# Kernel tuning notes

Hardware: AMD Instinct MI355X
Metric: run time of the kernel (lower is better)

The kernel has to match this reference:

```python
import jax, jax.numpy as jnp
import numpy as np

B, S, D = 4, 1024, 768
H = 12
DK = D // H            # 64
NUM_EMB = 10
MAX_DIST = 100000.0 * 2 ** 0.5
POS_SCALE = 100000.0   # tile positions live in [0, 100000]


def setup_inputs() -> dict:
    key = jax.random.key(0)
    ks = jax.random.split(key, 12)
    query = jax.random.normal(ks[0], (B, S, D), dtype=jnp.float32)
    key_t = jax.random.normal(ks[1], (B, S, D), dtype=jnp.float32)
    value = jax.random.normal(ks[2], (B, S, D), dtype=jnp.float32)
    tile_positions = jax.random.uniform(ks[3], (B, S, 2), dtype=jnp.float32) * POS_SCALE
    # Linear weights, torch layout [out, in]; xavier_uniform init, zero bias
    lim = float(np.sqrt(6.0 / (D + D)))
    Wq = jax.random.uniform(ks[4], (D, D), minval=-lim, maxval=lim, dtype=jnp.float32)
    Wk = jax.random.uniform(ks[5], (D, D), minval=-lim, maxval=lim, dtype=jnp.float32)
    Wv = jax.random.uniform(ks[6], (D, D), minval=-lim, maxval=lim, dtype=jnp.float32)
    bq = jnp.zeros((D,), jnp.float32)
    bk = jnp.zeros((D,), jnp.float32)
    bv = jnp.zeros((D,), jnp.float32)
    emb_k = jax.random.normal(ks[7], (NUM_EMB, DK), dtype=jnp.float32)  # nn.Embedding default N(0,1)
    return {"query": query, "key": key_t, "value": value,
            "tile_positions": tile_positions,
            "Wq": Wq, "bq": bq, "Wk": Wk, "bk": bk, "Wv": Wv, "bv": bv,
            "emb_k": emb_k}


def reference(query, key, value, tile_positions, Wq, bq, Wk, bk, Wv, bv, emb_k):
    b, s, _ = query.shape
    # projections -> [B, H, S, DK]
    q = (query @ Wq.T + bq).reshape(b, s, H, DK).transpose(0, 2, 1, 3)
    k = (key   @ Wk.T + bk).reshape(b, s, H, DK).transpose(0, 2, 1, 3)
    v = (value @ Wv.T + bv).reshape(b, s, H, DK).transpose(0, 2, 1, 3)
    # pairwise distances, normalized, discretized to embedding indices
    pos = jax.lax.stop_gradient(tile_positions)
    diff = pos[:, :, None, :] - pos[:, None, :, :]          # [B,S,S,2]
    dist = jnp.sqrt(jnp.sum(diff * diff, axis=-1)) / MAX_DIST  # [B,S,S]
    idx = jnp.clip(jnp.round(dist * (NUM_EMB - 1)), 0, NUM_EMB - 1).astype(jnp.int32)
    rk = emb_k[idx]                                          # [B,S,S,DK]
    # logits: QK^T plus distance-aware key bias
    attn_logits = jnp.einsum('bhqd,bhkd->bhqk', q, k)
    attn_logits = attn_logits + jnp.einsum('bhqd,bqkd->bhqk', q, rk)
    attn_logits = attn_logits / (DK ** 0.5)
    attention = jax.nn.softmax(attn_logits, axis=-1)
    out = jnp.einsum('bhqk,bhkd->bhqd', attention, v)       # [B,H,S,DK]
    out = out.transpose(0, 2, 1, 3).reshape(b, s, -1)       # [B,S,D]
    return out
```

## Files before the change

### kernel.cpp

```cpp
#include <hip/hip_runtime.h>
#include <hip/hip_bf16.h>

#define Bsz 4
#define Ssz 1024
#define Dsz 768
#define Hn 12
#define DKsz 64
#define NUMEMB 10

#define IDX_OFF 64
#define K_OFF   4194368
#define V_OFF   10485824
#define WBF_OFF 16777280
#define XBF_OFF 20316224
#define WS_TIER_B 20316224ULL
#define WS_TIER_A 39190592ULL

#define NXz 3145728
#define NWz 589824

#define KVBUF 4096

typedef __attribute__((ext_vector_type(8))) short short8;
typedef __attribute__((ext_vector_type(8))) float float8;
typedef __attribute__((ext_vector_type(4))) float f32x4;
typedef __attribute__((ext_vector_type(4))) unsigned int u32x4;
typedef __attribute__((ext_vector_type(2))) unsigned int u32x2;
typedef __attribute__((ext_vector_type(4))) short s16x4;

__device__ __forceinline__ float bfbits2f(short u) {
    union { unsigned int i; float f; } v;
    v.i = ((unsigned int)(unsigned short)u) << 16;
    return v.f;
}
__device__ __forceinline__ unsigned short f2bf_bits(float f) {
    __hip_bfloat16 h = __float2bfloat16(f);
    return *reinterpret_cast<unsigned short*>(&h);
}

__device__ __forceinline__ int dtvote(const unsigned int* p, int n) {
    int cnt = 0;
    for (int i = (threadIdx.x & 63); i < n; i += 64) {
        const unsigned int ex = (p[i] >> 7) & 0xFF;
        cnt += (ex >= 110 && ex <= 145) ? 1 : 0;
    }
#pragma unroll
    for (int off = 1; off < 64; off <<= 1) cnt += __shfl_xor(cnt, off, 64);
    return (2 * cnt > n) ? 1 : 0;
}

template<bool BF16>
__device__ __forceinline__ float loadf(const void* base, size_t idx) {
    if constexpr (BF16) return __bfloat162float(((const __hip_bfloat16*)base)[idx]);
    else return ((const float*)base)[idx];
}
template<bool BF16>
__device__ __forceinline__ short8 load8bf(const void* base, size_t idx) {
    if constexpr (BF16) {
        return *(const short8*)((const short*)base + idx);
    } else {
        float8 f = *(const float8*)((const float*)base + idx);
        short8 r;
#pragma unroll
        for (int i = 0; i < 8; i++) r[i] = (short)f2bf_bits(f[i]);
        return r;
    }
}
template<bool BF16>
__device__ __forceinline__ float8 load8f(const void* base, size_t idx) {
    if constexpr (BF16) {
        short8 s = *(const short8*)((const short*)base + idx);
        float8 f;
#pragma unroll
        for (int i = 0; i < 8; i++) f[i] = bfbits2f(s[i]);
        return f;
    } else {
        return *(const float8*)((const float*)base + idx);
    }
}

template<bool PB>
__device__ __forceinline__ void idx_body(
    const void* pos, unsigned char* __restrict__ idxb, int kt, int qt, int b)
{
    const int t = threadIdx.x;
    const int r = t >> 2, cc = t & 3;
    const int q = qt * 64 + r;
    const float qx = loadf<PB>(pos, ((size_t)b * Ssz + q) * 2);
    const float qy = loadf<PB>(pos, ((size_t)b * Ssz + q) * 2 + 1);
    const float MAXD = 141421.35623730951f;
    const int k0 = kt * 64 + cc * 16;
    unsigned int w[4];
#pragma unroll
    for (int g = 0; g < 4; g++) {
        unsigned int acc = 0;
#pragma unroll
        for (int u = 0; u < 4; u++) {
            const int k = k0 + g * 4 + u;
            const float kx = loadf<PB>(pos, ((size_t)b * Ssz + k) * 2);
            const float ky = loadf<PB>(pos, ((size_t)b * Ssz + k) * 2 + 1);
            const float dx = __fsub_rn(qx, kx);
            const float dy = __fsub_rn(qy, ky);
            const float ss = __fadd_rn(__fmul_rn(dx, dx), __fmul_rn(dy, dy));
            const float dist = __fdiv_rn(sqrtf(ss), MAXD);
            const float d9 = __fmul_rn(dist, 9.0f);
            int idx = (int)rintf(d9);
            idx = idx < 0 ? 0 : (idx > NUMEMB - 1 ? NUMEMB - 1 : idx);
            acc |= ((unsigned int)idx) << (8 * u);
        }
        w[g] = acc;
    }
    u32x4 v; v[0] = w[0]; v[1] = w[1]; v[2] = w[2]; v[3] = w[3];
    *(u32x4*)(idxb + ((size_t)(b * Ssz + q)) * Ssz + k0) = v;
}

__global__ __launch_bounds__(64) void detect_kernel(
    const unsigned int* __restrict__ q, const unsigned int* __restrict__ p,
    const unsigned int* __restrict__ w, const unsigned int* __restrict__ e,
    int* __restrict__ flags)
{
    const int which = blockIdx.x;
    const unsigned int* ptr = (which == 0) ? q : ((which == 1) ? p : ((which == 2) ? w : e));
    const int n = (which == 3) ? 320 : ((which == 1) ? 4096 : 1024);
    const int f = dtvote(ptr, n);
    if (threadIdx.x == 0) flags[which] = f;
}

__global__ __launch_bounds__(256) void idx_kernel(
    const void* pos, const int* __restrict__ flags, unsigned char* __restrict__ idxb)
{
    if (flags[1] != 0) idx_body<true >(pos, idxb, blockIdx.x, blockIdx.y, blockIdx.z);
    else               idx_body<false>(pos, idxb, blockIdx.x, blockIdx.y, blockIdx.z);
}

__global__ __launch_bounds__(256) void prep_kernel(
    const void* __restrict__ X0, const void* __restrict__ X1, const void* __restrict__ X2,
    const void* __restrict__ W0, const void* __restrict__ W1, const void* __restrict__ W2,
    const void* __restrict__ tpos, const void* __restrict__ emb,
    int* __restrict__ flags, short* __restrict__ Xbf, short* __restrict__ Wbf,
    unsigned char* __restrict__ idxb, int nconv, int doX)
{
    if ((int)blockIdx.x >= nconv) {
        const int i = blockIdx.x - nconv;
        const int kt = i & 15, qt = (i >> 4) & 15, b = i >> 8;
        const int pb = dtvote((const unsigned int*)tpos, 1024);
        if (pb) idx_body<true >(tpos, idxb, kt, qt, b);
        else    idx_body<false>(tpos, idxb, kt, qt, b);
        return;
    }

    if (blockIdx.x == 1) {
        const int f = dtvote((const unsigned int*)tpos, 1024);
        if (threadIdx.x == 0) flags[1] = f;
    } else if (blockIdx.x == 3) {
        const int f = dtvote((const unsigned int*)emb, 320);
        if (threadIdx.x == 0) flags[3] = f;
    }
    const bool xb = dtvote((const unsigned int*)X0, 256) != 0;
    const bool wb = dtvote((const unsigned int*)W0, 256) != 0;
    if (blockIdx.x == 0 && threadIdx.x == 0) { flags[0] = xb ? 1 : 0; flags[2] = wb ? 1 : 0; }

    const long t = (long)blockIdx.x * 256 + threadIdx.x;
    if (doX) {
        const long i8 = t * 8;
        if (i8 < (long)3 * NXz) {
            const int z = (int)(i8 / NXz);
            const long off = i8 - (long)z * NXz;
            const void* X = (z == 0) ? X0 : ((z == 1) ? X1 : X2);
            short8 v = xb ? load8bf<true>(X, off) : load8bf<false>(X, off);
            *(short8*)(Xbf + i8) = v;
        } else {
            const long j = i8 - (long)3 * NXz;
            const int z = (int)(j / NWz);
            const long off = j - (long)z * NWz;
            const void* W = (z == 0) ? W0 : ((z == 1) ? W1 : W2);
            short8 v = wb ? load8bf<true>(W, off) : load8bf<false>(W, off);
            *(short8*)(Wbf + j) = v;
        }
    } else {
        const long j = t * 8;
        const int z = (int)(j / NWz);
        const long off = j - (long)z * NWz;
        const void* W = (z == 0) ? W0 : ((z == 1) ? W1 : W2);
        short8 v = wb ? load8bf<true>(W, off) : load8bf<false>(W, off);
        *(short8*)(Wbf + j) = v;
    }
}

template<bool XB, bool WB>
__device__ __forceinline__ void proj_body(
    const void* X, const void* W, const void* bias, bool biasbf, void* Y, bool ybf,
    int zmode, int bx, int by, short* As, short* Bs)
{
    const int tid  = threadIdx.x;
    const int wave = tid >> 6;
    const int lane = tid & 63;
    const int l15  = lane & 15;
    const int quad = lane >> 4;
    const int wm = wave & 1;
    const int wn = wave >> 1;
    const int m0 = bx * 64;
    const int n0 = by * 128;

    f32x4 acc[2][4];
#pragma unroll
    for (int i = 0; i < 2; i++)
#pragma unroll
        for (int j = 0; j < 4; j++) acc[i][j] = (f32x4)0.0f;

    const int r0 = tid >> 3;
    const int cc = tid & 7;

    short8 pa0 = load8bf<XB>(X, (size_t)(m0 + r0)      * Dsz + cc * 8);
    short8 pa1 = load8bf<XB>(X, (size_t)(m0 + 32 + r0) * Dsz + cc * 8);
    short8 pb0 = load8bf<WB>(W, (size_t)(n0 + r0)      * Dsz + cc * 8);
    short8 pb1 = load8bf<WB>(W, (size_t)(n0 + 32 + r0) * Dsz + cc * 8);
    short8 pb2 = load8bf<WB>(W, (size_t)(n0 + 64 + r0) * Dsz + cc * 8);
    short8 pb3 = load8bf<WB>(W, (size_t)(n0 + 96 + r0) * Dsz + cc * 8);

    for (int kk = 0; kk < Dsz; kk += 64) {
        __syncthreads();
        *(short8*)&As[(r0)      * 72 + cc * 8] = pa0;
        *(short8*)&As[(32 + r0) * 72 + cc * 8] = pa1;
        *(short8*)&Bs[(r0)      * 72 + cc * 8] = pb0;
        *(short8*)&Bs[(32 + r0) * 72 + cc * 8] = pb1;
        *(short8*)&Bs[(64 + r0) * 72 + cc * 8] = pb2;
        *(short8*)&Bs[(96 + r0) * 72 + cc * 8] = pb3;
        __syncthreads();

        if (kk + 64 < Dsz) {
            const int k2 = kk + 64 + cc * 8;
            pa0 = load8bf<XB>(X, (size_t)(m0 + r0)      * Dsz + k2);
            pa1 = load8bf<XB>(X, (size_t)(m0 + 32 + r0) * Dsz + k2);
            pb0 = load8bf<WB>(W, (size_t)(n0 + r0)      * Dsz + k2);
            pb1 = load8bf<WB>(W, (size_t)(n0 + 32 + r0) * Dsz + k2);
            pb2 = load8bf<WB>(W, (size_t)(n0 + 64 + r0) * Dsz + k2);
            pb3 = load8bf<WB>(W, (size_t)(n0 + 96 + r0) * Dsz + k2);
        }

#pragma unroll
        for (int st = 0; st < 2; st++) {
            short8 af[2], bf[4];
#pragma unroll
            for (int i = 0; i < 2; i++)
                af[i] = *(const short8*)&As[(wm * 32 + i * 16 + l15) * 72 + st * 32 + quad * 8];
#pragma unroll
            for (int j = 0; j < 4; j++)
                bf[j] = *(const short8*)&Bs[(wn * 64 + j * 16 + l15) * 72 + st * 32 + quad * 8];
#pragma unroll
            for (int i = 0; i < 2; i++)
#pragma unroll
                for (int j = 0; j < 4; j++)
                    acc[i][j] = __builtin_amdgcn_mfma_f32_16x16x32_bf16(af[i], bf[j], acc[i][j], 0, 0, 0);
        }
    }

#pragma unroll
    for (int j = 0; j < 4; j++) {
        const int n = n0 + wn * 64 + j * 16 + l15;
        const float bv_ = biasbf ? loadf<true>(bias, n) : loadf<false>(bias, n);
        const int hh = n >> 6, dk = n & 63;
#pragma unroll
        for (int i = 0; i < 2; i++) {
            const int ms = m0 + wm * 32 + i * 16 + quad * 4;
            const int bb = ms >> 10;
            const int s0 = ms & 1023;
            if (zmode == 2) {
                s16x4 pkv;
#pragma unroll
                for (int r = 0; r < 4; r++) pkv[r] = (short)f2bf_bits(acc[i][j][r] + bv_);
                *(s16x4*)((short*)Y + (((size_t)bb * Hn + hh) * DKsz + dk) * Ssz + s0) = pkv;
            } else if (zmode == 1) {
#pragma unroll
                for (int r = 0; r < 4; r++)
                    ((__hip_bfloat16*)Y)[(((size_t)bb * Hn + hh) * Ssz + (s0 + r)) * DKsz + dk] =
                        __float2bfloat16(acc[i][j][r] + bv_);
            } else {
#pragma unroll
                for (int r = 0; r < 4; r++) {
                    const float val = acc[i][j][r] + bv_;
                    const size_t oi = (size_t)(ms + r) * Dsz + n;
                    if (ybf) ((__hip_bfloat16*)Y)[oi] = __float2bfloat16(val);
                    else     ((float*)Y)[oi] = val;
                }
            }
        }
    }
}

__global__ __launch_bounds__(256) void proj_kernel(
    const void* X0, const void* X1, const void* X2,
    const void* Wq, const void* bq, const void* Wk, const void* bk,
    const void* Wv, const void* bv,
    void* Qw, void* Kw, void* Vw, const int* __restrict__ flags,
    int fx, int fw)
{
    __shared__ __align__(16) short As[64 * 72];
    __shared__ __align__(16) short Bs[128 * 72];
    const int z = blockIdx.z;
    const void* X = (z == 0) ? X0 : ((z == 1) ? X1 : X2);
    const void* W = (z == 0) ? Wq : ((z == 1) ? Wk : Wv);
    const void* B = (z == 0) ? bq : ((z == 1) ? bk : bv);
    void* Y = (z == 0) ? Qw : ((z == 1) ? Kw : Vw);
    const bool xb = fx || flags[0] != 0;
    const bool wb = fw || flags[2] != 0;
    const bool biasbf = flags[2] != 0;
    const bool ybf = (flags[0] != 0) || (z != 0);
    if (xb) { if (wb) proj_body<true , true >(X, W, B, biasbf, Y, ybf, z, blockIdx.x, blockIdx.y, As, Bs);
              else    proj_body<true , false>(X, W, B, biasbf, Y, ybf, z, blockIdx.x, blockIdx.y, As, Bs); }
    else    { if (wb) proj_body<false, true >(X, W, B, biasbf, Y, ybf, z, blockIdx.x, blockIdx.y, As, Bs);
              else    proj_body<false, false>(X, W, B, biasbf, Y, ybf, z, blockIdx.x, blockIdx.y, As, Bs); }
}

template<bool QB, bool EB>
__device__ __forceinline__ void attn_body(
    const void* Qw, const short* __restrict__ Ks, const short* __restrict__ Vs,
    const unsigned char* __restrict__ idxb, const void* __restrict__ emb, void* out,
    unsigned short* Klds, unsigned short* Vtlds, float* qe)
{
    const int linear = blockIdx.x + 16 * (blockIdx.y + Hn * blockIdx.z);
    const int work = (linear & 7) * 96 + (linear >> 3);
    const int qt = work & 15;
    const int bh = work >> 4;
    const int h = bh % Hn;
    const int b = bh / Hn;

    const int tid  = threadIdx.x;
    const int wave = tid >> 6;
    const int lane = tid & 63;
    const int l15  = lane & 15;
    const int quad = lane >> 4;

    const float CSC = 0.18033688011112042f;

    for (int p = tid; p < 64 * NUMEMB; p += 256) {
        const int row = p / NUMEMB, e = p - row * NUMEMB;
        const size_t qoff = ((size_t)b * Ssz + qt * 64 + row) * Dsz + h * DKsz;
        float s = 0.f;
#pragma unroll
        for (int c = 0; c < 8; c++) {
            short8 qv = load8bf<QB>(Qw, qoff + c * 8);
            float8 ef = load8f<EB>(emb, (size_t)e * DKsz + c * 8);
#pragma unroll
            for (int i = 0; i < 8; i++) s += bfbits2f(qv[i]) * ef[i];
        }
        qe[p] = s * CSC;
    }

    short8 qfrag[2];
    {
        const size_t qbase = ((size_t)b * Ssz + qt * 64 + wave * 16 + l15) * Dsz + h * DKsz;
        qfrag[0] = load8bf<QB>(Qw, qbase + quad * 8);
        qfrag[1] = load8bf<QB>(Qw, qbase + 32 + quad * 8);
    }

    float m_run = -1e30f, l_run = 0.f;
    f32x4 oacc[4];
#pragma unroll
    for (int j = 0; j < 4; j++) oacc[j] = (f32x4)0.0f;

    const int r0 = tid >> 3, cc = tid & 7;
    const int swr   = (r0 & 3) | (((r0 >> 3) & 1) << 2);
    const int wroff = r0 * 64 + (cc ^ swr) * 8;

    const int swk = (l15 & 3) | (((l15 >> 2) & 1) << 2);
    const int vsw = (l15 & 3) | (((l15 >> 3) & 1) << 2);
    int koff[4][2];
#pragma unroll
    for (int jb = 0; jb < 4; jb++) {
        const int krow = (jb & 2) * 16 + (l15 >> 2) * 8 + (jb & 1) * 4 + (l15 & 3);
#pragma unroll
        for (int st = 0; st < 2; st++)
            koff[jb][st] = krow * 64 + ((st * 4 + quad) ^ swk) * 8;
    }
    int voff[2];
#pragma unroll
    for (int st = 0; st < 2; st++) voff[st] = ((st * 4 + quad) ^ vsw) * 8;

    const short* kp = Ks + ((size_t)(b * Hn + h) * Ssz) * DKsz + tid * 8;
    const short* vp = Vs + ((size_t)(b * Hn + h) * DKsz + r0) * Ssz + cc * 8;
    const unsigned char* ip = idxb + ((size_t)b * Ssz + qt * 64 + wave * 16 + l15) * Ssz + quad * 8;
    const int qrow10 = (wave * 16 + l15) * NUMEMB;

    short8 pk0 = *(const short8*)(kp);
    short8 pk1 = *(const short8*)(kp + 2048);
    short8 pv0 = *(const short8*)(vp);
    short8 pv1 = *(const short8*)(vp + 32 * Ssz);
    u32x2 idA = *(const u32x2*)(ip);
    u32x2 idB = *(const u32x2*)(ip + 32);

    *(short8*)&Klds[wroff]            = pk0;
    *(short8*)&Klds[32 * 64 + wroff]  = pk1;
    *(short8*)&Vtlds[wroff]           = pv0;
    *(short8*)&Vtlds[32 * 64 + wroff] = pv1;
    __syncthreads();

    for (int it = 0; it < 16; ++it) {
        const int cur = (it & 1) * KVBUF;
        const int nxt = cur ^ KVBUF;
        const unsigned int jd[4] = { idA[0], idA[1], idB[0], idB[1] };

        if (it + 1 < 16) {
            kp += 4096;
            vp += 64;
            ip += 64;
            pk0 = *(const short8*)(kp);
            pk1 = *(const short8*)(kp + 2048);
            pv0 = *(const short8*)(vp);
            pv1 = *(const short8*)(vp + 32 * Ssz);
            idA = *(const u32x2*)(ip);
            idB = *(const u32x2*)(ip + 32);
        }

        f32x4 sf[4];
#pragma unroll
        for (int jb = 0; jb < 4; jb++) sf[jb] = (f32x4)0.0f;
        __builtin_amdgcn_s_setprio(1);
#pragma unroll
        for (int st = 0; st < 2; st++) {
#pragma unroll
            for (int jb = 0; jb < 4; jb++) {
                short8 kf = *(const short8*)&Klds[cur + koff[jb][st]];
                sf[jb] = __builtin_amdgcn_mfma_f32_16x16x32_bf16(kf, qfrag[st], sf[jb], 0, 0, 0);
            }
        }
        __builtin_amdgcn_s_setprio(0);

        float sv[4][4];
#pragma unroll
        for (int jb = 0; jb < 4; jb++) {
            const unsigned int iw = jd[jb];
#pragma unroll
            for (int r = 0; r < 4; r++)
                sv[jb][r] = fmaf(sf[jb][r], CSC, qe[qrow10 + ((iw >> (8 * r)) & 0xFF)]);
        }

        float t0 = fmaxf(fmaxf(sv[0][0], sv[0][1]), fmaxf(sv[0][2], sv[0][3]));
        float t1 = fmaxf(fmaxf(sv[1][0], sv[1][1]), fmaxf(sv[1][2], sv[1][3]));
        float t2 = fmaxf(fmaxf(sv[2][0], sv[2][1]), fmaxf(sv[2][2], sv[2][3]));
        float t3 = fmaxf(fmaxf(sv[3][0], sv[3][1]), fmaxf(sv[3][2], sv[3][3]));
        float vmax = fmaxf(fmaxf(t0, t1), fmaxf(t2, t3));
        vmax = fmaxf(vmax, __shfl_xor(vmax, 16, 64));
        vmax = fmaxf(vmax, __shfl_xor(vmax, 32, 64));

        if (!__all(vmax - m_run <= 8.0f)) {
            const float mnew = fmaxf(m_run, vmax);
            const float alpha = exp2f(m_run - mnew);
            m_run = mnew;
            l_run *= alpha;
            float aO[4];
#pragma unroll
            for (int r = 0; r < 4; r++)
                aO[r] = __shfl(alpha, (lane & 48) | (quad * 4 + r), 64);
#pragma unroll
            for (int j = 0; j < 4; j++) {
                f32x4 o = oacc[j];
#pragma unroll
                for (int r = 0; r < 4; r++) o[r] *= aO[r];
                oacc[j] = o;
            }
        }

#pragma unroll
        for (int jb = 0; jb < 4; jb++)
#pragma unroll
            for (int r = 0; r < 4; r++)
                sv[jb][r] = exp2f(sv[jb][r] - m_run);

        float s0 = (sv[0][0] + sv[0][1]) + (sv[0][2] + sv[0][3]);
        float s1 = (sv[1][0] + sv[1][1]) + (sv[1][2] + sv[1][3]);
        float s2 = (sv[2][0] + sv[2][1]) + (sv[2][2] + sv[2][3]);
        float s3 = (sv[3][0] + sv[3][1]) + (sv[3][2] + sv[3][3]);
        float psum = (s0 + s1) + (s2 + s3);
        psum += __shfl_xor(psum, 16, 64);
        psum += __shfl_xor(psum, 32, 64);
        l_run += psum;

        short8 pa[2];
#pragma unroll
        for (int st = 0; st < 2; st++)
#pragma unroll
            for (int j = 0; j < 8; j++)
                pa[st][j] = (short)f2bf_bits(sv[2 * st + (j >> 2)][j & 3]);

        __builtin_amdgcn_s_setprio(1);
#pragma unroll
        for (int st = 0; st < 2; st++) {
#pragma unroll
            for (int j = 0; j < 4; j++) {
                short8 vb = *(const short8*)&Vtlds[cur + (j * 16 + l15) * 64 + voff[st]];
                oacc[j] = __builtin_amdgcn_mfma_f32_16x16x32_bf16(pa[st], vb, oacc[j], 0, 0, 0);
            }
        }
        __builtin_amdgcn_s_setprio(0);

        if (it + 1 < 16) {
            *(short8*)&Klds[nxt + wroff]            = pk0;
            *(short8*)&Klds[nxt + 32 * 64 + wroff]  = pk1;
            *(short8*)&Vtlds[nxt + wroff]           = pv0;
            *(short8*)&Vtlds[nxt + 32 * 64 + wroff] = pv1;
        }
        __syncthreads();
    }

    const float inv = 1.0f / l_run;
    float invO[4];
#pragma unroll
    for (int r = 0; r < 4; r++)
        invO[r] = __shfl(inv, (lane & 48) | (quad * 4 + r), 64);

#pragma unroll
    for (int r = 0; r < 4; r++) {
        const int m = qt * 64 + wave * 16 + quad * 4 + r;
#pragma unroll
        for (int j = 0; j < 4; j++) {
            const int n = h * DKsz + j * 16 + l15;
            const float val = oacc[j][r] * invO[r];
            const size_t oidx = ((size_t)b * Ssz + m) * Dsz + n;
            if constexpr (QB) ((__hip_bfloat16*)out)[oidx] = __float2bfloat16(val);
            else              ((float*)out)[oidx] = val;
        }
    }
}

__global__ __launch_bounds__(256) void attn_kernel(
    const void* Qw, const short* __restrict__ Ks, const short* __restrict__ Vs,
    const unsigned char* __restrict__ idxb, const void* __restrict__ emb, void* out,
    const int* __restrict__ flags)
{
    __shared__ __align__(16) unsigned short Klds[2 * KVBUF];
    __shared__ __align__(16) unsigned short Vtlds[2 * KVBUF];
    __shared__ __align__(16) float qe[64 * NUMEMB];

    const bool qb = flags[0] != 0, eb = flags[3] != 0;
    if (qb) { if (eb) attn_body<true , true >(Qw, Ks, Vs, idxb, emb, out, Klds, Vtlds, qe);
              else    attn_body<true , false>(Qw, Ks, Vs, idxb, emb, out, Klds, Vtlds, qe); }
    else    { if (eb) attn_body<false, true >(Qw, Ks, Vs, idxb, emb, out, Klds, Vtlds, qe);
              else    attn_body<false, false>(Qw, Ks, Vs, idxb, emb, out, Klds, Vtlds, qe); }
}

extern "C" void kernel_launch(void* const* d_in, const int* in_sizes, int n_in,
                              void* d_out, int out_size, void* d_ws, size_t ws_size,
                              hipStream_t stream) {
    const void* query = d_in[0];
    const void* key   = d_in[1];
    const void* value = d_in[2];
    const void* tpos  = d_in[3];
    const void* Wq    = d_in[4];
    const void* bq    = d_in[5];
    const void* Wk    = d_in[6];
    const void* bk    = d_in[7];
    const void* Wv    = d_in[8];
    const void* bv    = d_in[9];
    const void* emb   = d_in[10];

    int*           flags = (int*)d_ws;
    unsigned char* idxb  = (unsigned char*)d_ws + IDX_OFF;
    void*          Kw    = (char*)d_ws + K_OFF;
    void*          Vw    = (char*)d_ws + V_OFF;
    short*         Wbf   = (short*)((char*)d_ws + WBF_OFF);
    short*         Xbf   = (short*)((char*)d_ws + XBF_OFF);
    void*          Qw    = d_out;

    const bool tierA = ws_size >= WS_TIER_A;
    const bool tierB = !tierA && ws_size >= WS_TIER_B;

    if (tierA) {
        prep_kernel<<<5472 + 1024, 256, 0, stream>>>(
            query, key, value, Wq, Wk, Wv, tpos, emb,
            flags, Xbf, Wbf, idxb, 5472, 1);
        proj_kernel<<<dim3(64, 6, 3), 256, 0, stream>>>(
            Xbf, Xbf + NXz, Xbf + 2 * NXz,
            Wbf, bq, Wbf + NWz, bk, Wbf + 2 * NWz, bv,
            Qw, Kw, Vw, flags, 1, 1);
    } else if (tierB) {
        prep_kernel<<<864 + 1024, 256, 0, stream>>>(
            query, key, value, Wq, Wk, Wv, tpos, emb,
            flags, Xbf, Wbf, idxb, 864, 0);
        proj_kernel<<<dim3(64, 6, 3), 256, 0, stream>>>(
            query, key, value,
            Wbf, bq, Wbf + NWz, bk, Wbf + 2 * NWz, bv,
            Qw, Kw, Vw, flags, 0, 1);
    } else {
        detect_kernel<<<4, 64, 0, stream>>>(
            (const unsigned int*)query, (const unsigned int*)tpos,
            (const unsigned int*)Wq, (const unsigned int*)emb, flags);
        idx_kernel<<<dim3(16, 16, Bsz), 256, 0, stream>>>(tpos, flags, idxb);
        proj_kernel<<<dim3(64, 6, 3), 256, 0, stream>>>(
            query, key, value, Wq, bq, Wk, bk, Wv, bv,
            Qw, Kw, Vw, flags, 0, 0);
    }

    attn_kernel<<<dim3(16, Hn, Bsz), 256, 0, stream>>>(
        Qw, (const short*)Kw, (const short*)Vw, idxb, emb, d_out, flags);
}
```

Measured before the change: 200.9 us.

## Split attention KV range across two wave groups with LDS merge

The attention block grows to 512 threads, split into two groups of four waves. Each group processes half of the key/value sequence, so a block runs 8 iterations instead of 16. The groups merge their partial online-softmax state (max, sum, output) through shared memory in a final combine step. Double buffering is replaced by single-buffered per-group LDS with two barriers per iteration. The change trades per-block latency against the extra merge work, the extra synchronisation, and the loss of load/compute overlap.

```diff
diff --git a/kernel.cpp b/kernel.cpp
--- a/kernel.cpp
+++ b/kernel.cpp
@@ -19,7 +19,7 @@
 #define NXz 3145728
 #define NWz 589824
 
-#define KVBUF 4096
+#define POOLSZ 17664
 
 typedef __attribute__((ext_vector_type(8))) short short8;
 typedef __attribute__((ext_vector_type(8))) float float8;
@@ -316,7 +316,7 @@
 __device__ __forceinline__ void attn_body(
     const void* Qw, const short* __restrict__ Ks, const short* __restrict__ Vs,
     const unsigned char* __restrict__ idxb, const void* __restrict__ emb, void* out,
-    unsigned short* Klds, unsigned short* Vtlds, float* qe)
+    unsigned short* pool)
 {
     const int linear = blockIdx.x + 16 * (blockIdx.y + Hn * blockIdx.z);
     const int work = (linear & 7) * 96 + (linear >> 3);
@@ -327,13 +327,19 @@
 
     const int tid  = threadIdx.x;
     const int wave = tid >> 6;
+    const int g    = wave >> 2;
+    const int wv   = wave & 3;
     const int lane = tid & 63;
     const int l15  = lane & 15;
     const int quad = lane >> 4;
 
+    unsigned short* Klds  = pool + g * 8192;
+    unsigned short* Vtlds = pool + g * 8192 + 4096;
+    float* qe = (float*)(pool + 16384);
+
     const float CSC = 0.18033688011112042f;
 
-    for (int p = tid; p < 64 * NUMEMB; p += 256) {
+    for (int p = tid; p < 64 * NUMEMB; p += 512) {
         const int row = p / NUMEMB, e = p - row * NUMEMB;
         const size_t qoff = ((size_t)b * Ssz + qt * 64 + row) * Dsz + h * DKsz;
         float s = 0.f;
@@ -349,7 +355,7 @@
 
     short8 qfrag[2];
     {
-        const size_t qbase = ((size_t)b * Ssz + qt * 64 + wave * 16 + l15) * Dsz + h * DKsz;
+        const size_t qbase = ((size_t)b * Ssz + qt * 64 + wv * 16 + l15) * Dsz + h * DKsz;
         qfrag[0] = load8bf<QB>(Qw, qbase + quad * 8);
         qfrag[1] = load8bf<QB>(Qw, qbase + 32 + quad * 8);
     }
@@ -359,7 +365,8 @@
 #pragma unroll
     for (int j = 0; j < 4; j++) oacc[j] = (f32x4)0.0f;
 
-    const int r0 = tid >> 3, cc = tid & 7;
+    const int tg = tid & 255;
+    const int r0 = tg >> 3, cc = tg & 7;
     const int swr   = (r0 & 3) | (((r0 >> 3) & 1) << 2);
     const int wroff = r0 * 64 + (cc ^ swr) * 8;
 
@@ -377,10 +384,11 @@
 #pragma unroll
     for (int st = 0; st < 2; st++) voff[st] = ((st * 4 + quad) ^ vsw) * 8;
 
-    const short* kp = Ks + ((size_t)(b * Hn + h) * Ssz) * DKsz + tid * 8;
-    const short* vp = Vs + ((size_t)(b * Hn + h) * DKsz + r0) * Ssz + cc * 8;
-    const unsigned char* ip = idxb + ((size_t)b * Ssz + qt * 64 + wave * 16 + l15) * Ssz + quad * 8;
-    const int qrow10 = (wave * 16 + l15) * NUMEMB;
+    const short* kp = Ks + ((size_t)(b * Hn + h) * Ssz + g * 512) * DKsz + tg * 8;
+    const short* vp = Vs + ((size_t)(b * Hn + h) * DKsz + r0) * Ssz + g * 512 + cc * 8;
+    const unsigned char* ip = idxb + ((size_t)b * Ssz + qt * 64 + wv * 16 + l15) * Ssz
+                                   + g * 512 + quad * 8;
+    const int qrow10 = (wv * 16 + l15) * NUMEMB;
 
     short8 pk0 = *(const short8*)(kp);
     short8 pk1 = *(const short8*)(kp + 2048);
@@ -393,14 +401,12 @@
     *(short8*)&Klds[32 * 64 + wroff]  = pk1;
     *(short8*)&Vtlds[wroff]           = pv0;
     *(short8*)&Vtlds[32 * 64 + wroff] = pv1;
-    __syncthreads();
-
-    for (int it = 0; it < 16; ++it) {
-        const int cur = (it & 1) * KVBUF;
-        const int nxt = cur ^ KVBUF;
+
+    for (int it = 0; it < 8; ++it) {
+        __syncthreads();
         const unsigned int jd[4] = { idA[0], idA[1], idB[0], idB[1] };
 
-        if (it + 1 < 16) {
+        if (it + 1 < 8) {
             kp += 4096;
             vp += 64;
             ip += 64;
@@ -420,7 +426,7 @@
         for (int st = 0; st < 2; st++) {
 #pragma unroll
             for (int jb = 0; jb < 4; jb++) {
-                short8 kf = *(const short8*)&Klds[cur + koff[jb][st]];
+                short8 kf = *(const short8*)&Klds[koff[jb][st]];
                 sf[jb] = __builtin_amdgcn_mfma_f32_16x16x32_bf16(kf, qfrag[st], sf[jb], 0, 0, 0);
             }
         }
@@ -488,55 +494,80 @@
         for (int st = 0; st < 2; st++) {
 #pragma unroll
             for (int j = 0; j < 4; j++) {
-                short8 vb = *(const short8*)&Vtlds[cur + (j * 16 + l15) * 64 + voff[st]];
+                short8 vb = *(const short8*)&Vtlds[(j * 16 + l15) * 64 + voff[st]];
                 oacc[j] = __builtin_amdgcn_mfma_f32_16x16x32_bf16(pa[st], vb, oacc[j], 0, 0, 0);
             }
         }
         __builtin_amdgcn_s_setprio(0);
 
-        if (it + 1 < 16) {
-            *(short8*)&Klds[nxt + wroff]            = pk0;
-            *(short8*)&Klds[nxt + 32 * 64 + wroff]  = pk1;
-            *(short8*)&Vtlds[nxt + wroff]           = pv0;
-            *(short8*)&Vtlds[nxt + 32 * 64 + wroff] = pv1;
-        }
         __syncthreads();
-    }
-
-    const float inv = 1.0f / l_run;
-    float invO[4];
-#pragma unroll
-    for (int r = 0; r < 4; r++)
-        invO[r] = __shfl(inv, (lane & 48) | (quad * 4 + r), 64);
-
-#pragma unroll
-    for (int r = 0; r < 4; r++) {
-        const int m = qt * 64 + wave * 16 + quad * 4 + r;
-#pragma unroll
-        for (int j = 0; j < 4; j++) {
-            const int n = h * DKsz + j * 16 + l15;
-            const float val = oacc[j][r] * invO[r];
-            const size_t oidx = ((size_t)b * Ssz + m) * Dsz + n;
-            if constexpr (QB) ((__hip_bfloat16*)out)[oidx] = __float2bfloat16(val);
-            else              ((float*)out)[oidx] = val;
-        }
-    }
-}
-
-__global__ __launch_bounds__(256) void attn_kernel(
+
+        if (it + 1 < 8) {
+            *(short8*)&Klds[wroff]            = pk0;
+            *(short8*)&Klds[32 * 64 + wroff]  = pk1;
+            *(short8*)&Vtlds[wroff]           = pv0;
+            *(short8*)&Vtlds[32 * 64 + wroff] = pv1;
+        }
+    }
+
+    __syncthreads();
+    float* Ob = (float*)pool;
+    float* mB = (float*)(pool + 8192);
+    float* lB = mB + 64;
+
+    if (g == 1) {
+        if (quad == 0) { mB[wv * 16 + l15] = m_run; lB[wv * 16 + l15] = l_run; }
+#pragma unroll
+        for (int r = 0; r < 4; r++)
+#pragma unroll
+            for (int j = 0; j < 4; j++)
+                Ob[(wv * 16 + quad * 4 + r) * 64 + j * 16 + l15] = oacc[j][r];
+    }
+    __syncthreads();
+
+    if (g == 0) {
+        const float mBv = mB[wv * 16 + l15];
+        const float lBv = lB[wv * 16 + l15];
+        const float ms  = fmaxf(m_run, mBv);
+        const float aA  = exp2f(m_run - ms);
+        const float aB  = exp2f(mBv - ms);
+        const float inv = 1.0f / (l_run * aA + lBv * aB);
+        const float fA  = aA * inv;
+        const float fB  = aB * inv;
+        float fAo[4], fBo[4];
+#pragma unroll
+        for (int r = 0; r < 4; r++) {
+            fAo[r] = __shfl(fA, (lane & 48) | (quad * 4 + r), 64);
+            fBo[r] = __shfl(fB, (lane & 48) | (quad * 4 + r), 64);
+        }
+#pragma unroll
+        for (int r = 0; r < 4; r++) {
+            const int m = qt * 64 + wv * 16 + quad * 4 + r;
+#pragma unroll
+            for (int j = 0; j < 4; j++) {
+                const int n = h * DKsz + j * 16 + l15;
+                const float ob = Ob[(wv * 16 + quad * 4 + r) * 64 + j * 16 + l15];
+                const float val = oacc[j][r] * fAo[r] + ob * fBo[r];
+                const size_t oidx = ((size_t)b * Ssz + m) * Dsz + n;
+                if constexpr (QB) ((__hip_bfloat16*)out)[oidx] = __float2bfloat16(val);
+                else              ((float*)out)[oidx] = val;
+            }
+        }
+    }
+}
+
+__global__ __launch_bounds__(512) void attn_kernel(
     const void* Qw, const short* __restrict__ Ks, const short* __restrict__ Vs,
     const unsigned char* __restrict__ idxb, const void* __restrict__ emb, void* out,
     const int* __restrict__ flags)
 {
-    __shared__ __align__(16) unsigned short Klds[2 * KVBUF];
-    __shared__ __align__(16) unsigned short Vtlds[2 * KVBUF];
-    __shared__ __align__(16) float qe[64 * NUMEMB];
+    __shared__ __align__(16) unsigned short pool[POOLSZ];
 
     const bool qb = flags[0] != 0, eb = flags[3] != 0;
-    if (qb) { if (eb) attn_body<true , true >(Qw, Ks, Vs, idxb, emb, out, Klds, Vtlds, qe);
-              else    attn_body<true , false>(Qw, Ks, Vs, idxb, emb, out, Klds, Vtlds, qe); }
-    else    { if (eb) attn_body<false, true >(Qw, Ks, Vs, idxb, emb, out, Klds, Vtlds, qe);
-              else    attn_body<false, false>(Qw, Ks, Vs, idxb, emb, out, Klds, Vtlds, qe); }
+    if (qb) { if (eb) attn_body<true , true >(Qw, Ks, Vs, idxb, emb, out, pool);
+              else    attn_body<true , false>(Qw, Ks, Vs, idxb, emb, out, pool); }
+    else    { if (eb) attn_body<false, true >(Qw, Ks, Vs, idxb, emb, out, pool);
+              else    attn_body<false, false>(Qw, Ks, Vs, idxb, emb, out, pool); }
 }
 
 extern "C" void kernel_launch(void* const* d_in, const int* in_sizes, int n_in,
@@ -591,6 +622,6 @@
             Qw, Kw, Vw, flags, 0, 0);
     }
 
-    attn_kernel<<<dim3(16, Hn, Bsz), 256, 0, stream>>>(
+    attn_kernel<<<dim3(16, Hn, Bsz), 512, 0, stream>>>(
         Qw, (const short*)Kw, (const short*)Vw, idxb, emb, d_out, flags);
 }
```

Result: no change. 202.8 us (+1.0%).
